# Kernel optimization log

Hardware: AMD Instinct MI355X
Metric: run time of the kernel (lower is better)

Reference implementation:

```python
import jax, jax.numpy as jnp
import numpy as np
from jax import lax

B, N, C, H, W, D, BEV = 2, 6, 64, 128, 352, 48, 64


def _make_buffers():
    # depths: linspace(1,100,D) -> used with shape (1,1,D,1)
    depths = jnp.linspace(1.0, 100.0, D).reshape(1, 1, D, 1)
    y, x = jnp.meshgrid(jnp.arange(H), jnp.arange(W), indexing='ij')
    xy1 = jnp.stack((x.flatten(), y.flatten(), jnp.ones(H * W)), axis=0).astype(jnp.float32)  # (3, H*W)
    return depths, xy1


def setup_inputs() -> dict:
    key = jax.random.key(0)
    ks = jax.random.split(key, 8)
    image_features = jax.random.normal(ks[0], (B * N, C, H, W), jnp.float32)
    # realistic invertible pinhole intrinsics embedded in 4x4
    fx = 500.0 + 10.0 * jax.random.normal(ks[1], (B, N))
    fy = 500.0 + 10.0 * jax.random.normal(ks[2], (B, N))
    K = jnp.tile(jnp.eye(4, dtype=jnp.float32), (B, N, 1, 1))
    K = K.at[..., 0, 0].set(fx).at[..., 1, 1].set(fy)
    K = K.at[..., 0, 2].set(W / 2.0).at[..., 1, 2].set(H / 2.0)
    extrinsics = jnp.tile(jnp.eye(4, dtype=jnp.float32), (B, N, 1, 1)) + 0.01 * jax.random.normal(ks[3], (B, N, 4, 4))
    view_attention = jnp.ones((1, N, 1, H, W), jnp.float32)
    depth_attention = jnp.ones((1, D, 1, 1), jnp.float32)
    # kaiming-normal conv weights (fan_in mode, relu gain sqrt(2))
    c1w = jax.random.normal(ks[4], (BEV, 3, 3, 3), jnp.float32) * np.sqrt(2.0 / (3 * 9))
    c1b = jnp.zeros((BEV,), jnp.float32)
    c2w = jax.random.normal(ks[5], (BEV, BEV, 3, 3), jnp.float32) * np.sqrt(2.0 / (BEV * 9))
    c2b = jnp.zeros((BEV,), jnp.float32)
    bn1_g = jnp.ones((BEV,), jnp.float32); bn1_b = jnp.zeros((BEV,), jnp.float32)
    bn2_g = jnp.ones((BEV,), jnp.float32); bn2_b = jnp.zeros((BEV,), jnp.float32)
    depths, xy1 = _make_buffers()
    return dict(image_features=image_features, intrinsics=K, extrinsics=extrinsics,
                view_attention=view_attention, depth_attention=depth_attention,
                c1w=c1w, c1b=c1b, bn1_g=bn1_g, bn1_b=bn1_b,
                c2w=c2w, c2b=c2b, bn2_g=bn2_g, bn2_b=bn2_b,
                depths=depths, xy1=xy1)


def _conv3x3(x, w, b):
    y = lax.conv_general_dilated(x, w, (1, 1), 'SAME',
                                 dimension_numbers=('NCHW', 'OIHW', 'NCHW'))
    return y + b.reshape(1, -1, 1, 1)


def _bn_train(x, g, b, eps=1e-5):
    # torch BatchNorm2d in training mode: biased batch stats over (B,H,W)
    m = x.mean(axis=(0, 2, 3), keepdims=True)
    v = x.var(axis=(0, 2, 3), keepdims=True)
    return g.reshape(1, -1, 1, 1) * (x - m) * lax.rsqrt(v + eps) + b.reshape(1, -1, 1, 1)


def reference(image_features, intrinsics, extrinsics, view_attention, depth_attention,
              c1w, c1b, bn1_g, bn1_b, c2w, c2b, bn2_g, bn2_b, depths, xy1):
    BN = B * N
    # ---- lift ----
    K3 = intrinsics.reshape(BN, 4, 4)[:, :3, :3]
    Kinv = jnp.linalg.inv(K3)                          # (BN,3,3)
    rays = jnp.einsum('bij,jp->bip', Kinv, xy1)        # (BN,3,H*W)
    # depths (1,1,D,1) * rays (BN,3,1,HW) -> (BN,3,D,HW), then the original's
    # .view(B,N,3,H,W,D) (a raw row-major reshape, reproduced faithfully)
    pc = (depths * rays[:, :, None, :]).reshape(B, N, 3, H, W, D)
    # (depth_probs in the original is computed then discarded; omitted)
    # ---- splat (fused weighted reduction over N and D) ----
    da = jax.nn.softmax(depth_attention, axis=1).reshape(D)       # (D,)
    va = jax.nn.softmax(view_attention, axis=1)[0, :, 0]          # (N,H,W)
    bev_features = jnp.einsum('bnchwd,d,nhw->bchw', pc, da, va)   # (B,3,H,W)
    h = jax.nn.relu(_bn_train(_conv3x3(bev_features, c1w, c1b), bn1_g, bn1_b))
    bev = jax.nn.relu(_bn_train(_conv3x3(h, c2w, c2b), bn2_g, bn2_b))
    return pc, bev
```

## Files before the change

### kernel.cpp

```cpp
#include <hip/hip_runtime.h>

#define W_ 352
#define H_ 128
#define HW 45056
#define D_ 48
#define B_ 2
#define N_ 6
#define DHW (D_*HW)
#define PC_SIZE (36*DHW)
#define BHW (B_*HW)
#define BEVN (B_*64*HW)

#define WS_KINV 0
#define WS_SUM1 192
#define WS_SQ1  256
#define WS_SUM2 448
#define WS_SQ2  512

#define NBN_BLK (BEVN/2048)
#define NPC_BLK (PC_SIZE/1024)

typedef unsigned short ushort_t;
typedef __attribute__((ext_vector_type(8))) short bf16x8;
typedef __attribute__((ext_vector_type(4))) float f32x4;
typedef __attribute__((ext_vector_type(8))) unsigned short u16x8;

static __device__ inline ushort_t f2bf(float f) {
    union { float f; unsigned u; } v; v.f = f;
    unsigned r = v.u + 0x7FFF + ((v.u >> 16) & 1);
    return (ushort_t)(r >> 16);
}
static __device__ inline float bf2f(ushort_t u) {
    union { unsigned u; float f; } v; v.u = ((unsigned)u) << 16; return v.f;
}
static __device__ inline void invert3x3(const float* __restrict__ M, float* __restrict__ o) {
    float a = M[0], b = M[1], c = M[2];
    float d = M[4], e = M[5], f = M[6];
    float g = M[8], h = M[9], ii = M[10];
    float det = a*(e*ii - f*h) - b*(d*ii - f*g) + c*(d*h - e*g);
    float inv = 1.f / det;
    o[0] = (e*ii - f*h)*inv; o[1] = (c*h - b*ii)*inv; o[2] = (b*f - c*e)*inv;
    o[3] = (f*g - d*ii)*inv; o[4] = (a*ii - c*g)*inv; o[5] = (c*d - a*f)*inv;
    o[6] = (d*h - e*g)*inv;  o[7] = (b*g - a*h)*inv;  o[8] = (a*e - b*d)*inv;
}

__global__ __launch_bounds__(256) void k_bevf(const float* __restrict__ K4,
                                              const float* __restrict__ datt,
                                              const float* __restrict__ vatt,
                                              const float* __restrict__ depths,
                                              float* __restrict__ ws,
                                              float* __restrict__ bevf) {
    int t = threadIdx.x;
    if (blockIdx.x == 176) {
        for (int i = 192 + t; i < 640; i += 256) ws[i] = 0.f;
        if (t < 12) invert3x3(K4 + t * 16, ws + WS_KINV + t * 9);
        return;
    }
    __shared__ float sKinv[108], sDa[48], sDep[48];
    if (t < 48) sDep[t] = depths[t];
    if (t >= 192 && t < 204) invert3x3(K4 + (t - 192) * 16, sKinv + (t - 192) * 9);
    if (t == 255) {
        float mx = -1e30f;
        for (int k = 0; k < D_; k++) mx = fmaxf(mx, datt[k]);
        float s = 0.f, e[D_];
        for (int k = 0; k < D_; k++) { e[k] = expf(datt[k] - mx); s += e[k]; }
        float invs = 1.f / s;
        for (int k = 0; k < D_; k++) sDa[k] = e[k] * invs;
    }
    __syncthreads();
    int pix = blockIdx.x * 256 + t;
    float va[N_]; float mx = -1e30f;
    for (int n = 0; n < N_; n++) { va[n] = vatt[n * HW + pix]; mx = fmaxf(mx, va[n]); }
    float s = 0.f;
    for (int n = 0; n < N_; n++) { va[n] = expf(va[n] - mx); s += va[n]; }
    float invs = 1.f / s;
    int q0 = pix * 48;
    int d = q0 / HW;
    int p = q0 - d * HW;
    int y = p / W_;
    int x = p - y * W_;
    float fx = (float)x, fy = (float)y;
    float S0 = 0.f, S1 = 0.f, S2 = 0.f;
    #pragma unroll
    for (int dd = 0; dd < D_; dd++) {
        float wq = sDa[dd] * sDep[d];
        S0 = fmaf(wq, fx, S0);
        S1 = fmaf(wq, fy, S1);
        S2 += wq;
        x++; fx += 1.f;
        if (x == W_) { x = 0; fx = 0.f; y++; fy += 1.f; if (y == H_) { y = 0; fy = 0.f; d++; } }
    }
    for (int b = 0; b < B_; b++) {
        float a0 = 0.f, a1 = 0.f, a2 = 0.f;
        for (int n = 0; n < N_; n++) {
            float van = va[n] * invs;
            const float* kv = sKinv + (b * N_ + n) * 9;
            a0 = fmaf(van, fmaf(kv[0], S0, fmaf(kv[1], S1, kv[2] * S2)), a0);
            a1 = fmaf(van, fmaf(kv[3], S0, fmaf(kv[4], S1, kv[5] * S2)), a1);
            a2 = fmaf(van, fmaf(kv[6], S0, fmaf(kv[7], S1, kv[8] * S2)), a2);
        }
        bevf[(b * 3 + 0) * HW + pix] = a0;
        bevf[(b * 3 + 1) * HW + pix] = a1;
        bevf[(b * 3 + 2) * HW + pix] = a2;
    }
}

__global__ __launch_bounds__(256) void k_conv1(const float* __restrict__ bevf,
                                               const float* __restrict__ w1,
                                               const float* __restrict__ b1,
                                               const float* __restrict__ w2,
                                               ushort_t* __restrict__ h1pm,
                                               ushort_t* __restrict__ packedW) {
    if (blockIdx.x >= 352) {
        int e = (blockIdx.x - 352) * 256 + threadIdx.x;
        int tap = e >> 12;
        int r   = e & 4095;
        int n   = r >> 6, k = r & 63;
        int slot = (k >> 3) ^ (n & 7);
        packedW[tap * 4096 + n * 64 + slot * 8 + (k & 7)] = f2bf(w2[(n * 64 + k) * 9 + tap]);
        return;
    }
    __shared__ float wl[64 * 27];
    for (int i = threadIdx.x; i < 64 * 27; i += 256) wl[i] = w1[i];
    __syncthreads();
    int pix = blockIdx.x * 256 + threadIdx.x;
    int b = pix / HW;
    int rem = pix - b * HW;
    int h = rem / W_;
    int w = rem - h * W_;
    float v[27];
    #pragma unroll
    for (int ci = 0; ci < 3; ci++)
        #pragma unroll
        for (int dy = 0; dy < 3; dy++)
            #pragma unroll
            for (int dx = 0; dx < 3; dx++) {
                int hh = h + dy - 1, ww = w + dx - 1;
                float val = 0.f;
                if (hh >= 0 && hh < H_ && ww >= 0 && ww < W_)
                    val = bevf[(b * 3 + ci) * HW + hh * W_ + ww];
                v[ci * 9 + dy * 3 + dx] = val;
            }
    u16x8 pack[8];
    #pragma unroll
    for (int co = 0; co < 64; co++) {
        float acc = b1[co];
        #pragma unroll
        for (int k = 0; k < 27; k++) acc = fmaf(wl[co * 27 + k], v[k], acc);
        pack[co >> 3][co & 7] = (short)f2bf(acc);
    }
    ushort_t* dst = h1pm + pix * 64;
    #pragma unroll
    for (int j = 0; j < 8; j++)
        *(u16x8*)(dst + j * 8) = pack[j];
}

__global__ __launch_bounds__(256) void k_stats(const ushort_t* __restrict__ x,
                                               float* __restrict__ ws) {
    __shared__ float sSum[64], sSq[64];
    int tid = threadIdx.x;
    if (tid < 64) { sSum[tid] = 0.f; sSq[tid] = 0.f; }
    __syncthreads();
    int c8 = tid & 7;
    int lp = tid >> 3;
    int base = blockIdx.x * 352;
    float s[8] = {0,0,0,0,0,0,0,0}, q[8] = {0,0,0,0,0,0,0,0};
    for (int p = lp; p < 352; p += 32) {
        u16x8 v = *(const u16x8*)(x + (base + p) * 64 + c8 * 8);
        #pragma unroll
        for (int e = 0; e < 8; e++) {
            float f = bf2f(v[e]);
            s[e] += f;
            q[e] = fmaf(f, f, q[e]);
        }
    }
    #pragma unroll
    for (int e = 0; e < 8; e++) {
        s[e] += __shfl_xor(s[e], 8);  s[e] += __shfl_xor(s[e], 16); s[e] += __shfl_xor(s[e], 32);
        q[e] += __shfl_xor(q[e], 8);  q[e] += __shfl_xor(q[e], 16); q[e] += __shfl_xor(q[e], 32);
    }
    if ((tid & 56) == 0) {
        #pragma unroll
        for (int e = 0; e < 8; e++) {
            atomicAdd(&sSum[c8 * 8 + e], s[e]);
            atomicAdd(&sSq[c8 * 8 + e], q[e]);
        }
    }
    __syncthreads();
    if (tid < 64) {
        atomicAdd(ws + WS_SUM1 + tid, sSum[tid]);
        atomicAdd(ws + WS_SQ1 + tid, sSq[tid]);
    }
}

__global__ __launch_bounds__(256) void k_conv2(const ushort_t* __restrict__ h1pm,
                                               const ushort_t* __restrict__ packedW,
                                               const float* __restrict__ b2,
                                               const float* __restrict__ g1,
                                               const float* __restrict__ bb1,
                                               float* __restrict__ ws,
                                               float* __restrict__ h2f) {
    __shared__ __align__(16) ushort_t sA[204 * 64];
    __shared__ __align__(16) ushort_t sB[3 * 4096];
    __shared__ float sSc[64], sSh[64];
    __shared__ float sRs[4][64], sRq[4][64];

    const int tid = threadIdx.x;
    if (tid < 64) {
        const float invM = 1.f / (float)BHW;
        float m = ws[WS_SUM1 + tid] * invM;
        float var = ws[WS_SQ1 + tid] * invM - m * m;
        float sc = g1[tid] * rsqrtf(var + 1e-5f);
        sSc[tid] = sc;
        sSh[tid] = bb1[tid] - m * sc;
    }
    __syncthreads();

    const int b  = blockIdx.z;
    const int x0 = blockIdx.x * 32;
    const int y0 = blockIdx.y * 4;
    const ushort_t* h1p = h1pm + b * HW * 64;

    for (int idx = tid; idx < 204 * 8; idx += 256) {
        int r  = idx >> 3;
        int c8 = idx & 7;
        int hy = r / 34;
        int hx = r - hy * 34;
        int py = y0 + hy - 1, px = x0 + hx - 1;
        u16x8 ov = {0, 0, 0, 0, 0, 0, 0, 0};
        if ((unsigned)py < H_ && (unsigned)px < W_) {
            u16x8 v = *(const u16x8*)(h1p + (py * W_ + px) * 64 + c8 * 8);
            #pragma unroll
            for (int e = 0; e < 8; e++) {
                int ci = c8 * 8 + e;
                float f = fmaxf(fmaf(sSc[ci], bf2f(v[e]), sSh[ci]), 0.f);
                ov[e] = (short)f2bf(f);
            }
        }
        int slot = c8 ^ (r & 7);
        *(u16x8*)(&sA[r * 64 + slot * 8]) = ov;
    }

    const int w    = tid >> 6;
    const int lane = tid & 63;
    const int g    = lane >> 4;
    const int c16  = lane & 15;

    f32x4 acc[2][4];
    #pragma unroll
    for (int m = 0; m < 2; m++)
        #pragma unroll
        for (int n = 0; n < 4; n++)
            acc[m][n] = (f32x4){0.f, 0.f, 0.f, 0.f};

    for (int grp = 0; grp < 3; grp++) {
        __syncthreads();
        const uint4* src = (const uint4*)(packedW + grp * 3 * 4096);
        uint4* dst = (uint4*)sB;
        #pragma unroll
        for (int i = 0; i < 6; i++) dst[tid + 256 * i] = src[tid + 256 * i];
        __syncthreads();
        #pragma unroll
        for (int tt = 0; tt < 3; tt++) {
            bf16x8 afr[2][2];
            #pragma unroll
            for (int mrep = 0; mrep < 2; mrep++)
                #pragma unroll
                for (int kk = 0; kk < 2; kk++) {
                    int r = (w + grp) * 34 + tt + c16 + 16 * mrep;
                    int slot = (g + 4 * kk) ^ (r & 7);
                    afr[mrep][kk] = *(const bf16x8*)(&sA[r * 64 + slot * 8]);
                }
            #pragma unroll
            for (int nrep = 0; nrep < 4; nrep++) {
                int n = 16 * nrep + c16;
                #pragma unroll
                for (int kk = 0; kk < 2; kk++) {
                    int slot = (g + 4 * kk) ^ (n & 7);
                    bf16x8 bfr = *(const bf16x8*)(&sB[tt * 4096 + n * 64 + slot * 8]);
                    #pragma unroll
                    for (int mrep = 0; mrep < 2; mrep++)
                        acc[mrep][nrep] = __builtin_amdgcn_mfma_f32_16x16x32_bf16(
                            afr[mrep][kk], bfr, acc[mrep][nrep], 0, 0, 0);
                }
            }
        }
    }

    const int y = y0 + w;
    #pragma unroll
    for (int nrep = 0; nrep < 4; nrep++) {
        int co = 16 * nrep + c16;
        float bias = b2[co];
        float* dstrow = h2f + (b * 64 + co) * HW + y * W_;
        float s = 0.f, q = 0.f;
        #pragma unroll
        for (int mrep = 0; mrep < 2; mrep++)
            #pragma unroll
            for (int j = 0; j < 4; j++) {
                float val = acc[mrep][nrep][j] + bias;
                s += val;
                q = fmaf(val, val, q);
                dstrow[x0 + 16 * mrep + g * 4 + j] = val;
            }
        s += __shfl_xor(s, 16); s += __shfl_xor(s, 32);
        q += __shfl_xor(q, 16); q += __shfl_xor(q, 32);
        if (g == 0) { sRs[w][co] = s; sRq[w][co] = q; }
    }
    __syncthreads();
    if (tid < 64) {
        float s = sRs[0][tid] + sRs[1][tid] + sRs[2][tid] + sRs[3][tid];
        float q = sRq[0][tid] + sRq[1][tid] + sRq[2][tid] + sRq[3][tid];
        atomicAdd(ws + WS_SUM2 + tid, s);
        atomicAdd(ws + WS_SQ2 + tid, q);
    }
}

__global__ __launch_bounds__(256) void k_tail(const float* __restrict__ depths,
                                              const float* __restrict__ ws,
                                              const float* __restrict__ g2,
                                              const float* __restrict__ bb2,
                                              float* __restrict__ out) {
    int bid = blockIdx.x;
    if (bid < NBN_BLK) {
        float* bev = out + PC_SIZE;
        int t = bid * 256 + threadIdx.x;
        int f = t * 8;
        int c = (f / HW) & 63;
        const float invM = 1.f / (float)BHW;
        float m = ws[WS_SUM2 + c] * invM;
        float var = ws[WS_SQ2 + c] * invM - m * m;
        float sc = g2[c] * rsqrtf(var + 1e-5f);
        float sh = bb2[c] - m * sc;
        f32x4 a = *(f32x4*)(bev + f);
        f32x4 d = *(f32x4*)(bev + f + 4);
        a.x = fmaxf(fmaf(sc, a.x, sh), 0.f);
        a.y = fmaxf(fmaf(sc, a.y, sh), 0.f);
        a.z = fmaxf(fmaf(sc, a.z, sh), 0.f);
        a.w = fmaxf(fmaf(sc, a.w, sh), 0.f);
        d.x = fmaxf(fmaf(sc, d.x, sh), 0.f);
        d.y = fmaxf(fmaf(sc, d.y, sh), 0.f);
        d.z = fmaxf(fmaf(sc, d.z, sh), 0.f);
        d.w = fmaxf(fmaf(sc, d.w, sh), 0.f);
        *(f32x4*)(bev + f) = a;
        *(f32x4*)(bev + f + 4) = d;
    } else {
        int t = (bid - NBN_BLK) * 256 + threadIdx.x;
        int f = t * 4;
        int bnc = f / DHW;
        int r1  = f - bnc * DHW;
        int d   = r1 / HW;
        int p   = r1 - d * HW;
        int y   = p / W_;
        int x   = p - y * W_;
        float ka = ws[WS_KINV + bnc * 3 + 0];
        float kb = ws[WS_KINV + bnc * 3 + 1];
        float kc = ws[WS_KINV + bnc * 3 + 2];
        float dep = depths[d];
        float base = fmaf(kb, (float)y, kc);
        f32x4 v;
        v.x = dep * fmaf(ka, (float)(x + 0), base);
        v.y = dep * fmaf(ka, (float)(x + 1), base);
        v.z = dep * fmaf(ka, (float)(x + 2), base);
        v.w = dep * fmaf(ka, (float)(x + 3), base);
        __builtin_nontemporal_store(v, (f32x4*)(out + f));
    }
}

extern "C" void kernel_launch(void* const* d_in, const int* in_sizes, int n_in,
                              void* d_out, int out_size, void* d_ws, size_t ws_size,
                              hipStream_t stream) {
    const float* K4     = (const float*)d_in[1];
    const float* vatt   = (const float*)d_in[3];
    const float* datt   = (const float*)d_in[4];
    const float* c1w    = (const float*)d_in[5];
    const float* c1b    = (const float*)d_in[6];
    const float* g1     = (const float*)d_in[7];
    const float* bb1    = (const float*)d_in[8];
    const float* c2w    = (const float*)d_in[9];
    const float* c2b    = (const float*)d_in[10];
    const float* g2     = (const float*)d_in[11];
    const float* bb2    = (const float*)d_in[12];
    const float* depths = (const float*)d_in[13];

    float* out = (float*)d_out;
    float* ws  = (float*)d_ws;
    char* base = (char*)d_out;
    ushort_t* h1pm    = (ushort_t*)base;
    float*    bevf    = (float*)(base + (32u << 20));
    ushort_t* packedW = (ushort_t*)(base + (36u << 20));
    float*    h2f     = out + PC_SIZE;

    k_bevf<<<177, 256, 0, stream>>>(K4, datt, vatt, depths, ws, bevf);
    k_conv1<<<496, 256, 0, stream>>>(bevf, c1w, c1b, c2w, h1pm, packedW);
    k_stats<<<256, 256, 0, stream>>>(h1pm, ws);
    k_conv2<<<dim3(11, 32, 2), 256, 0, stream>>>(h1pm, packedW, c2b, g1, bb1, ws, h2f);
    k_tail<<<NBN_BLK + NPC_BLK, 256, 0, stream>>>(depths, ws, g2, bb2, out);
}
```

Measured before the change: 129.9 us.

## Spread point-cloud writes across all kernels to overlap with compute stages

The large point-cloud output write, previously done entirely in the final tail kernel, is split into chunks and appended as extra blocks to each of the five kernels. Each pc block inverts its camera's intrinsics itself, so it no longer depends on the workspace. Scratch buffers move into the last slice of the pc region, which the tail kernel writes last. The aim is to hide the memory-bound pc stores behind the compute-bound conv and stats stages, at the cost of redundant per-thread 3x3 inversions and bandwidth contention with those stages.

```diff
diff --git a/kernel.cpp b/kernel.cpp
--- a/kernel.cpp
+++ b/kernel.cpp
@@ -11,14 +11,19 @@
 #define BHW (B_*HW)
 #define BEVN (B_*64*HW)
 
-#define WS_KINV 0
 #define WS_SUM1 192
 #define WS_SQ1  256
 #define WS_SUM2 448
 #define WS_SQ2  512
 
 #define NBN_BLK (BEVN/2048)
-#define NPC_BLK (PC_SIZE/1024)
+#define SCRATCH_F 4194304
+#define PCA_TOT ((PC_SIZE - SCRATCH_F)/1024)
+#define PCA1 22000
+#define PCA2 20000
+#define PCA3 18000
+#define PCA4 (PCA_TOT - PCA1 - PCA2 - PCA3)
+#define TAILPC (SCRATCH_F/1024)
 
 typedef unsigned short ushort_t;
 typedef __attribute__((ext_vector_type(8))) short bf16x8;
@@ -44,16 +49,49 @@
     o[6] = (d*h - e*g)*inv;  o[7] = (b*g - a*h)*inv;  o[8] = (a*e - b*d)*inv;
 }
 
+static __device__ inline void pc_write(int pcblk, const float* __restrict__ K4,
+                                       const float* __restrict__ depths,
+                                       float* __restrict__ out) {
+    int f = pcblk * 1024 + (int)threadIdx.x * 4;
+    int bnc = f / DHW;
+    int r1  = f - bnc * DHW;
+    int d   = r1 / HW;
+    int p   = r1 - d * HW;
+    int y   = p / W_;
+    int x   = p - y * W_;
+    int bn  = bnc / 3;
+    int rr  = bnc - bn * 3;
+    const float* M = K4 + bn * 16;
+    float a = M[0], b = M[1], c = M[2];
+    float dd = M[4], e = M[5], ff = M[6];
+    float g = M[8], h = M[9], i = M[10];
+    float det = a*(e*i - ff*h) + b*(ff*g - dd*i) + c*(dd*h - e*g);
+    float inv = 1.f / det;
+    float ka, kb, kc;
+    if (rr == 0)      { ka = (e*i - ff*h)*inv;  kb = (c*h - b*i)*inv;  kc = (b*ff - c*e)*inv; }
+    else if (rr == 1) { ka = (ff*g - dd*i)*inv; kb = (a*i - c*g)*inv;  kc = (c*dd - a*ff)*inv; }
+    else              { ka = (dd*h - e*g)*inv;  kb = (b*g - a*h)*inv;  kc = (a*e - b*dd)*inv; }
+    float dep = depths[d];
+    float base = fmaf(kb, (float)y, kc);
+    f32x4 v;
+    v.x = dep * fmaf(ka, (float)(x + 0), base);
+    v.y = dep * fmaf(ka, (float)(x + 1), base);
+    v.z = dep * fmaf(ka, (float)(x + 2), base);
+    v.w = dep * fmaf(ka, (float)(x + 3), base);
+    __builtin_nontemporal_store(v, (f32x4*)(out + f));
+}
+
 __global__ __launch_bounds__(256) void k_bevf(const float* __restrict__ K4,
                                               const float* __restrict__ datt,
                                               const float* __restrict__ vatt,
                                               const float* __restrict__ depths,
                                               float* __restrict__ ws,
-                                              float* __restrict__ bevf) {
-    int t = threadIdx.x;
-    if (blockIdx.x == 176) {
+                                              float* __restrict__ bevf,
+                                              float* __restrict__ out) {
+    int bid = blockIdx.x, t = threadIdx.x;
+    if (bid >= 177) { pc_write(bid - 177, K4, depths, out); return; }
+    if (bid == 176) {
         for (int i = 192 + t; i < 640; i += 256) ws[i] = 0.f;
-        if (t < 12) invert3x3(K4 + t * 16, ws + WS_KINV + t * 9);
         return;
     }
     __shared__ float sKinv[108], sDa[48], sDep[48];
@@ -68,7 +106,7 @@
         for (int k = 0; k < D_; k++) sDa[k] = e[k] * invs;
     }
     __syncthreads();
-    int pix = blockIdx.x * 256 + t;
+    int pix = bid * 256 + t;
     float va[N_]; float mx = -1e30f;
     for (int n = 0; n < N_; n++) { va[n] = vatt[n * HW + pix]; mx = fmaxf(mx, va[n]); }
     float s = 0.f;
@@ -110,9 +148,14 @@
                                                const float* __restrict__ b1,
                                                const float* __restrict__ w2,
                                                ushort_t* __restrict__ h1pm,
-                                               ushort_t* __restrict__ packedW) {
-    if (blockIdx.x >= 352) {
-        int e = (blockIdx.x - 352) * 256 + threadIdx.x;
+                                               ushort_t* __restrict__ packedW,
+                                               const float* __restrict__ K4,
+                                               const float* __restrict__ depths,
+                                               float* __restrict__ out) {
+    int bid = blockIdx.x;
+    if (bid >= 496) { pc_write(bid - 496 + PCA1, K4, depths, out); return; }
+    if (bid >= 352) {
+        int e = (bid - 352) * 256 + threadIdx.x;
         int tap = e >> 12;
         int r   = e & 4095;
         int n   = r >> 6, k = r & 63;
@@ -123,7 +166,7 @@
     __shared__ float wl[64 * 27];
     for (int i = threadIdx.x; i < 64 * 27; i += 256) wl[i] = w1[i];
     __syncthreads();
-    int pix = blockIdx.x * 256 + threadIdx.x;
+    int pix = bid * 256 + threadIdx.x;
     int b = pix / HW;
     int rem = pix - b * HW;
     int h = rem / W_;
@@ -156,14 +199,19 @@
 }
 
 __global__ __launch_bounds__(256) void k_stats(const ushort_t* __restrict__ x,
-                                               float* __restrict__ ws) {
+                                               float* __restrict__ ws,
+                                               const float* __restrict__ K4,
+                                               const float* __restrict__ depths,
+                                               float* __restrict__ out) {
+    int bid = blockIdx.x;
+    if (bid >= 256) { pc_write(bid - 256 + PCA1 + PCA2, K4, depths, out); return; }
     __shared__ float sSum[64], sSq[64];
     int tid = threadIdx.x;
     if (tid < 64) { sSum[tid] = 0.f; sSq[tid] = 0.f; }
     __syncthreads();
     int c8 = tid & 7;
     int lp = tid >> 3;
-    int base = blockIdx.x * 352;
+    int base = bid * 352;
     float s[8] = {0,0,0,0,0,0,0,0}, q[8] = {0,0,0,0,0,0,0,0};
     for (int p = lp; p < 352; p += 32) {
         u16x8 v = *(const u16x8*)(x + (base + p) * 64 + c8 * 8);
@@ -199,7 +247,13 @@
                                                const float* __restrict__ g1,
                                                const float* __restrict__ bb1,
                                                float* __restrict__ ws,
-                                               float* __restrict__ h2f) {
+                                               float* __restrict__ h2f,
+                                               const float* __restrict__ K4,
+                                               const float* __restrict__ depths,
+                                               float* __restrict__ out) {
+    int bid = blockIdx.x;
+    if (bid >= 704) { pc_write(bid - 704 + PCA1 + PCA2 + PCA3, K4, depths, out); return; }
+
     __shared__ __align__(16) ushort_t sA[204 * 64];
     __shared__ __align__(16) ushort_t sB[3 * 4096];
     __shared__ float sSc[64], sSh[64];
@@ -216,9 +270,12 @@
     }
     __syncthreads();
 
-    const int b  = blockIdx.z;
-    const int x0 = blockIdx.x * 32;
-    const int y0 = blockIdx.y * 4;
+    const int b  = bid / 352;
+    const int r0 = bid - b * 352;
+    const int yb = r0 / 11;
+    const int xb = r0 - yb * 11;
+    const int x0 = xb * 32;
+    const int y0 = yb * 4;
     const ushort_t* h1p = h1pm + b * HW * 64;
 
     for (int idx = tid; idx < 204 * 8; idx += 256) {
@@ -320,51 +377,31 @@
                                               const float* __restrict__ ws,
                                               const float* __restrict__ g2,
                                               const float* __restrict__ bb2,
+                                              const float* __restrict__ K4,
                                               float* __restrict__ out) {
     int bid = blockIdx.x;
-    if (bid < NBN_BLK) {
-        float* bev = out + PC_SIZE;
-        int t = bid * 256 + threadIdx.x;
-        int f = t * 8;
-        int c = (f / HW) & 63;
-        const float invM = 1.f / (float)BHW;
-        float m = ws[WS_SUM2 + c] * invM;
-        float var = ws[WS_SQ2 + c] * invM - m * m;
-        float sc = g2[c] * rsqrtf(var + 1e-5f);
-        float sh = bb2[c] - m * sc;
-        f32x4 a = *(f32x4*)(bev + f);
-        f32x4 d = *(f32x4*)(bev + f + 4);
-        a.x = fmaxf(fmaf(sc, a.x, sh), 0.f);
-        a.y = fmaxf(fmaf(sc, a.y, sh), 0.f);
-        a.z = fmaxf(fmaf(sc, a.z, sh), 0.f);
-        a.w = fmaxf(fmaf(sc, a.w, sh), 0.f);
-        d.x = fmaxf(fmaf(sc, d.x, sh), 0.f);
-        d.y = fmaxf(fmaf(sc, d.y, sh), 0.f);
-        d.z = fmaxf(fmaf(sc, d.z, sh), 0.f);
-        d.w = fmaxf(fmaf(sc, d.w, sh), 0.f);
-        *(f32x4*)(bev + f) = a;
-        *(f32x4*)(bev + f + 4) = d;
-    } else {
-        int t = (bid - NBN_BLK) * 256 + threadIdx.x;
-        int f = t * 4;
-        int bnc = f / DHW;
-        int r1  = f - bnc * DHW;
-        int d   = r1 / HW;
-        int p   = r1 - d * HW;
-        int y   = p / W_;
-        int x   = p - y * W_;
-        float ka = ws[WS_KINV + bnc * 3 + 0];
-        float kb = ws[WS_KINV + bnc * 3 + 1];
-        float kc = ws[WS_KINV + bnc * 3 + 2];
-        float dep = depths[d];
-        float base = fmaf(kb, (float)y, kc);
-        f32x4 v;
-        v.x = dep * fmaf(ka, (float)(x + 0), base);
-        v.y = dep * fmaf(ka, (float)(x + 1), base);
-        v.z = dep * fmaf(ka, (float)(x + 2), base);
-        v.w = dep * fmaf(ka, (float)(x + 3), base);
-        __builtin_nontemporal_store(v, (f32x4*)(out + f));
-    }
+    if (bid >= NBN_BLK) { pc_write(bid - NBN_BLK + PCA_TOT, K4, depths, out); return; }
+    float* bev = out + PC_SIZE;
+    int t = bid * 256 + threadIdx.x;
+    int f = t * 8;
+    int c = (f / HW) & 63;
+    const float invM = 1.f / (float)BHW;
+    float m = ws[WS_SUM2 + c] * invM;
+    float var = ws[WS_SQ2 + c] * invM - m * m;
+    float sc = g2[c] * rsqrtf(var + 1e-5f);
+    float sh = bb2[c] - m * sc;
+    f32x4 a = *(f32x4*)(bev + f);
+    f32x4 d = *(f32x4*)(bev + f + 4);
+    a.x = fmaxf(fmaf(sc, a.x, sh), 0.f);
+    a.y = fmaxf(fmaf(sc, a.y, sh), 0.f);
+    a.z = fmaxf(fmaf(sc, a.z, sh), 0.f);
+    a.w = fmaxf(fmaf(sc, a.w, sh), 0.f);
+    d.x = fmaxf(fmaf(sc, d.x, sh), 0.f);
+    d.y = fmaxf(fmaf(sc, d.y, sh), 0.f);
+    d.z = fmaxf(fmaf(sc, d.z, sh), 0.f);
+    d.w = fmaxf(fmaf(sc, d.w, sh), 0.f);
+    *(f32x4*)(bev + f) = a;
+    *(f32x4*)(bev + f + 4) = d;
 }
 
 extern "C" void kernel_launch(void* const* d_in, const int* in_sizes, int n_in,
@@ -385,15 +422,15 @@
 
     float* out = (float*)d_out;
     float* ws  = (float*)d_ws;
-    char* base = (char*)d_out;
-    ushort_t* h1pm    = (ushort_t*)base;
-    float*    bevf    = (float*)(base + (32u << 20));
-    ushort_t* packedW = (ushort_t*)(base + (36u << 20));
+    char* sbase = (char*)d_out + (size_t)(PC_SIZE - SCRATCH_F) * 4;
+    ushort_t* h1pm    = (ushort_t*)sbase;
+    float*    bevf    = (float*)(sbase + (12u << 20));
+    ushort_t* packedW = (ushort_t*)(sbase + (14u << 20));
     float*    h2f     = out + PC_SIZE;
 
-    k_bevf<<<177, 256, 0, stream>>>(K4, datt, vatt, depths, ws, bevf);
-    k_conv1<<<496, 256, 0, stream>>>(bevf, c1w, c1b, c2w, h1pm, packedW);
-    k_stats<<<256, 256, 0, stream>>>(h1pm, ws);
-    k_conv2<<<dim3(11, 32, 2), 256, 0, stream>>>(h1pm, packedW, c2b, g1, bb1, ws, h2f);
-    k_tail<<<NBN_BLK + NPC_BLK, 256, 0, stream>>>(depths, ws, g2, bb2, out);
-}
+    k_bevf <<<177 + PCA1, 256, 0, stream>>>(K4, datt, vatt, depths, ws, bevf, out);
+    k_conv1<<<496 + PCA2, 256, 0, stream>>>(bevf, c1w, c1b, c2w, h1pm, packedW, K4, depths, out);
+    k_stats<<<256 + PCA3, 256, 0, stream>>>(h1pm, ws, K4, depths, out);
+    k_conv2<<<704 + PCA4, 256, 0, stream>>>(h1pm, packedW, c2b, g1, bb1, ws, h2f, K4, depths, out);
+    k_tail <<<NBN_BLK + TAILPC, 256, 0, stream>>>(depths, ws, g2, bb2, K4, out);
+}
```

Result: slower. 136.6 us (+5.2%).

## Fuse BEV feature computation into conv1 tiles and widen point-cloud stores

Applied to the files above, without the earlier changes.

The separate BEV-feature kernel is merged into the first convolution: each 8x32 tile computes its haloed BEV features directly into shared memory, so the bevf intermediate buffer and one launch go away. The point-cloud writer in the tail kernel now writes eight floats per thread and computes the K-inverse row inline instead of reading it from the workspace. Halo recomputation adds some redundant per-pixel softmax and depth-sum work, and conv2 switches to a flattened 1D grid.

```diff
diff --git a/kernel.cpp b/kernel.cpp
--- a/kernel.cpp
+++ b/kernel.cpp
@@ -11,14 +11,13 @@
 #define BHW (B_*HW)
 #define BEVN (B_*64*HW)
 
-#define WS_KINV 0
 #define WS_SUM1 192
 #define WS_SQ1  256
 #define WS_SUM2 448
 #define WS_SQ2  512
 
 #define NBN_BLK (BEVN/2048)
-#define NPC_BLK (PC_SIZE/1024)
+#define NPC_BLK (PC_SIZE/2048)
 
 typedef unsigned short ushort_t;
 typedef __attribute__((ext_vector_type(8))) short bf16x8;
@@ -44,22 +43,78 @@
     o[6] = (d*h - e*g)*inv;  o[7] = (b*g - a*h)*inv;  o[8] = (a*e - b*d)*inv;
 }
 
-__global__ __launch_bounds__(256) void k_bevf(const float* __restrict__ K4,
-                                              const float* __restrict__ datt,
-                                              const float* __restrict__ vatt,
-                                              const float* __restrict__ depths,
-                                              float* __restrict__ ws,
-                                              float* __restrict__ bevf) {
-    int t = threadIdx.x;
-    if (blockIdx.x == 176) {
-        for (int i = 192 + t; i < 640; i += 256) ws[i] = 0.f;
-        if (t < 12) invert3x3(K4 + t * 16, ws + WS_KINV + t * 9);
+static __device__ inline void pc_write8(int pcblk, const float* __restrict__ K4,
+                                        const float* __restrict__ depths,
+                                        float* __restrict__ out) {
+    int f = pcblk * 2048 + (int)threadIdx.x * 8;
+    int bnc = f / DHW;
+    int r1  = f - bnc * DHW;
+    int d   = r1 / HW;
+    int p   = r1 - d * HW;
+    int y   = p / W_;
+    int x   = p - y * W_;
+    int bn  = bnc / 3;
+    int rr  = bnc - bn * 3;
+    const float* M = K4 + bn * 16;
+    float a = M[0], b = M[1], c = M[2];
+    float dd = M[4], e = M[5], ff = M[6];
+    float g = M[8], h = M[9], i = M[10];
+    float det = a*(e*i - ff*h) + b*(ff*g - dd*i) + c*(dd*h - e*g);
+    float inv = 1.f / det;
+    float ka, kb, kc;
+    if (rr == 0)      { ka = (e*i - ff*h)*inv;  kb = (c*h - b*i)*inv;  kc = (b*ff - c*e)*inv; }
+    else if (rr == 1) { ka = (ff*g - dd*i)*inv; kb = (a*i - c*g)*inv;  kc = (c*dd - a*ff)*inv; }
+    else              { ka = (dd*h - e*g)*inv;  kb = (b*g - a*h)*inv;  kc = (a*e - b*dd)*inv; }
+    float dep = depths[d];
+    float base = fmaf(kb, (float)y, kc);
+    f32x4 v0, v1;
+    v0.x = dep * fmaf(ka, (float)(x + 0), base);
+    v0.y = dep * fmaf(ka, (float)(x + 1), base);
+    v0.z = dep * fmaf(ka, (float)(x + 2), base);
+    v0.w = dep * fmaf(ka, (float)(x + 3), base);
+    v1.x = dep * fmaf(ka, (float)(x + 4), base);
+    v1.y = dep * fmaf(ka, (float)(x + 5), base);
+    v1.z = dep * fmaf(ka, (float)(x + 6), base);
+    v1.w = dep * fmaf(ka, (float)(x + 7), base);
+    __builtin_nontemporal_store(v0, (f32x4*)(out + f));
+    __builtin_nontemporal_store(v1, (f32x4*)(out + f + 4));
+}
+
+__global__ __launch_bounds__(256) void k_fused1(const float* __restrict__ K4,
+                                                const float* __restrict__ datt,
+                                                const float* __restrict__ vatt,
+                                                const float* __restrict__ depths,
+                                                const float* __restrict__ w1,
+                                                const float* __restrict__ b1,
+                                                const float* __restrict__ w2,
+                                                float* __restrict__ ws,
+                                                ushort_t* __restrict__ h1pm,
+                                                ushort_t* __restrict__ packedW) {
+    int bid = blockIdx.x, tid = threadIdx.x;
+    if (bid >= 352) {
+        int e = (bid - 352) * 256 + tid;
+        int tap = e >> 12;
+        int r   = e & 4095;
+        int n   = r >> 6, k = r & 63;
+        int slot = (k >> 3) ^ (n & 7);
+        packedW[tap * 4096 + n * 64 + slot * 8 + (k & 7)] = f2bf(w2[(n * 64 + k) * 9 + tap]);
         return;
     }
-    __shared__ float sKinv[108], sDa[48], sDep[48];
-    if (t < 48) sDep[t] = depths[t];
-    if (t >= 192 && t < 204) invert3x3(K4 + (t - 192) * 16, sKinv + (t - 192) * 9);
-    if (t == 255) {
+    if (bid == 0) {
+        for (int i = 192 + tid; i < 576; i += 256) ws[i] = 0.f;
+    }
+    __shared__ float sBev[3][10][34];
+    __shared__ float wl[64 * 27];
+    __shared__ float sDep[48], sDa[48], sKinv[54];
+
+    int b  = bid / 176;
+    int t0 = bid - b * 176;
+    int ty = t0 / 11, tx = t0 - ty * 11;
+    int y0 = ty * 8, x0 = tx * 32;
+
+    if (tid < 48) sDep[tid] = depths[tid];
+    if (tid >= 64 && tid < 70) invert3x3(K4 + (b * 6 + tid - 64) * 16, sKinv + (tid - 64) * 9);
+    if (tid == 192) {
         float mx = -1e30f;
         for (int k = 0; k < D_; k++) mx = fmaxf(mx, datt[k]);
         float s = 0.f, e[D_];
@@ -67,80 +122,60 @@
         float invs = 1.f / s;
         for (int k = 0; k < D_; k++) sDa[k] = e[k] * invs;
     }
-    __syncthreads();
-    int pix = blockIdx.x * 256 + t;
-    float va[N_]; float mx = -1e30f;
-    for (int n = 0; n < N_; n++) { va[n] = vatt[n * HW + pix]; mx = fmaxf(mx, va[n]); }
-    float s = 0.f;
-    for (int n = 0; n < N_; n++) { va[n] = expf(va[n] - mx); s += va[n]; }
-    float invs = 1.f / s;
-    int q0 = pix * 48;
-    int d = q0 / HW;
-    int p = q0 - d * HW;
-    int y = p / W_;
-    int x = p - y * W_;
-    float fx = (float)x, fy = (float)y;
-    float S0 = 0.f, S1 = 0.f, S2 = 0.f;
-    #pragma unroll
-    for (int dd = 0; dd < D_; dd++) {
-        float wq = sDa[dd] * sDep[d];
-        S0 = fmaf(wq, fx, S0);
-        S1 = fmaf(wq, fy, S1);
-        S2 += wq;
-        x++; fx += 1.f;
-        if (x == W_) { x = 0; fx = 0.f; y++; fy += 1.f; if (y == H_) { y = 0; fy = 0.f; d++; } }
-    }
-    for (int b = 0; b < B_; b++) {
+    for (int i = tid; i < 64 * 27; i += 256) wl[i] = w1[i];
+    __syncthreads();
+
+    for (int idx = tid; idx < 340; idx += 256) {
+        int hy = idx / 34, hx = idx - hy * 34;
+        int py = y0 + hy - 1, px = x0 + hx - 1;
         float a0 = 0.f, a1 = 0.f, a2 = 0.f;
-        for (int n = 0; n < N_; n++) {
-            float van = va[n] * invs;
-            const float* kv = sKinv + (b * N_ + n) * 9;
-            a0 = fmaf(van, fmaf(kv[0], S0, fmaf(kv[1], S1, kv[2] * S2)), a0);
-            a1 = fmaf(van, fmaf(kv[3], S0, fmaf(kv[4], S1, kv[5] * S2)), a1);
-            a2 = fmaf(van, fmaf(kv[6], S0, fmaf(kv[7], S1, kv[8] * S2)), a2);
+        if ((unsigned)py < H_ && (unsigned)px < W_) {
+            int pix = py * W_ + px;
+            float va[N_]; float mx = -1e30f;
+            for (int n = 0; n < N_; n++) { va[n] = vatt[n * HW + pix]; mx = fmaxf(mx, va[n]); }
+            float s = 0.f;
+            for (int n = 0; n < N_; n++) { va[n] = expf(va[n] - mx); s += va[n]; }
+            float invs = 1.f / s;
+            int q0 = pix * 48;
+            int d = q0 / HW;
+            int p = q0 - d * HW;
+            int y = p / W_;
+            int x = p - y * W_;
+            float fx = (float)x, fy = (float)y;
+            float S0 = 0.f, S1 = 0.f, S2 = 0.f;
+            #pragma unroll
+            for (int dd = 0; dd < D_; dd++) {
+                float wq = sDa[dd] * sDep[d];
+                S0 = fmaf(wq, fx, S0);
+                S1 = fmaf(wq, fy, S1);
+                S2 += wq;
+                x++; fx += 1.f;
+                if (x == W_) { x = 0; fx = 0.f; y++; fy += 1.f; if (y == H_) { y = 0; fy = 0.f; d++; } }
+            }
+            for (int n = 0; n < N_; n++) {
+                float van = va[n] * invs;
+                const float* kv = sKinv + n * 9;
+                a0 = fmaf(van, fmaf(kv[0], S0, fmaf(kv[1], S1, kv[2] * S2)), a0);
+                a1 = fmaf(van, fmaf(kv[3], S0, fmaf(kv[4], S1, kv[5] * S2)), a1);
+                a2 = fmaf(van, fmaf(kv[6], S0, fmaf(kv[7], S1, kv[8] * S2)), a2);
+            }
         }
-        bevf[(b * 3 + 0) * HW + pix] = a0;
-        bevf[(b * 3 + 1) * HW + pix] = a1;
-        bevf[(b * 3 + 2) * HW + pix] = a2;
-    }
-}
-
-__global__ __launch_bounds__(256) void k_conv1(const float* __restrict__ bevf,
-                                               const float* __restrict__ w1,
-                                               const float* __restrict__ b1,
-                                               const float* __restrict__ w2,
-                                               ushort_t* __restrict__ h1pm,
-                                               ushort_t* __restrict__ packedW) {
-    if (blockIdx.x >= 352) {
-        int e = (blockIdx.x - 352) * 256 + threadIdx.x;
-        int tap = e >> 12;
-        int r   = e & 4095;
-        int n   = r >> 6, k = r & 63;
-        int slot = (k >> 3) ^ (n & 7);
-        packedW[tap * 4096 + n * 64 + slot * 8 + (k & 7)] = f2bf(w2[(n * 64 + k) * 9 + tap]);
-        return;
-    }
-    __shared__ float wl[64 * 27];
-    for (int i = threadIdx.x; i < 64 * 27; i += 256) wl[i] = w1[i];
-    __syncthreads();
-    int pix = blockIdx.x * 256 + threadIdx.x;
-    int b = pix / HW;
-    int rem = pix - b * HW;
-    int h = rem / W_;
-    int w = rem - h * W_;
+        sBev[0][hy][hx] = a0;
+        sBev[1][hy][hx] = a1;
+        sBev[2][hy][hx] = a2;
+    }
+    __syncthreads();
+
+    int oy = tid >> 5, ox = tid & 31;
+    int y = y0 + oy, x = x0 + ox;
     float v[27];
     #pragma unroll
     for (int ci = 0; ci < 3; ci++)
         #pragma unroll
         for (int dy = 0; dy < 3; dy++)
             #pragma unroll
-            for (int dx = 0; dx < 3; dx++) {
-                int hh = h + dy - 1, ww = w + dx - 1;
-                float val = 0.f;
-                if (hh >= 0 && hh < H_ && ww >= 0 && ww < W_)
-                    val = bevf[(b * 3 + ci) * HW + hh * W_ + ww];
-                v[ci * 9 + dy * 3 + dx] = val;
-            }
+            for (int dx = 0; dx < 3; dx++)
+                v[ci * 9 + dy * 3 + dx] = sBev[ci][oy + dy][ox + dx];
     u16x8 pack[8];
     #pragma unroll
     for (int co = 0; co < 64; co++) {
@@ -149,7 +184,7 @@
         for (int k = 0; k < 27; k++) acc = fmaf(wl[co * 27 + k], v[k], acc);
         pack[co >> 3][co & 7] = (short)f2bf(acc);
     }
-    ushort_t* dst = h1pm + pix * 64;
+    ushort_t* dst = h1pm + (size_t)(b * HW + y * W_ + x) * 64;
     #pragma unroll
     for (int j = 0; j < 8; j++)
         *(u16x8*)(dst + j * 8) = pack[j];
@@ -166,7 +201,7 @@
     int base = blockIdx.x * 352;
     float s[8] = {0,0,0,0,0,0,0,0}, q[8] = {0,0,0,0,0,0,0,0};
     for (int p = lp; p < 352; p += 32) {
-        u16x8 v = *(const u16x8*)(x + (base + p) * 64 + c8 * 8);
+        u16x8 v = *(const u16x8*)(x + (size_t)(base + p) * 64 + c8 * 8);
         #pragma unroll
         for (int e = 0; e < 8; e++) {
             float f = bf2f(v[e]);
@@ -216,10 +251,14 @@
     }
     __syncthreads();
 
-    const int b  = blockIdx.z;
-    const int x0 = blockIdx.x * 32;
-    const int y0 = blockIdx.y * 4;
-    const ushort_t* h1p = h1pm + b * HW * 64;
+    const int bid = blockIdx.x;
+    const int b  = bid / 352;
+    const int r0 = bid - b * 352;
+    const int yb = r0 / 11;
+    const int xb = r0 - yb * 11;
+    const int x0 = xb * 32;
+    const int y0 = yb * 4;
+    const ushort_t* h1p = h1pm + (size_t)b * HW * 64;
 
     for (int idx = tid; idx < 204 * 8; idx += 256) {
         int r  = idx >> 3;
@@ -229,7 +268,7 @@
         int py = y0 + hy - 1, px = x0 + hx - 1;
         u16x8 ov = {0, 0, 0, 0, 0, 0, 0, 0};
         if ((unsigned)py < H_ && (unsigned)px < W_) {
-            u16x8 v = *(const u16x8*)(h1p + (py * W_ + px) * 64 + c8 * 8);
+            u16x8 v = *(const u16x8*)(h1p + (size_t)(py * W_ + px) * 64 + c8 * 8);
             #pragma unroll
             for (int e = 0; e < 8; e++) {
                 int ci = c8 * 8 + e;
@@ -292,7 +331,7 @@
     for (int nrep = 0; nrep < 4; nrep++) {
         int co = 16 * nrep + c16;
         float bias = b2[co];
-        float* dstrow = h2f + (b * 64 + co) * HW + y * W_;
+        float* dstrow = h2f + (size_t)(b * 64 + co) * HW + y * W_;
         float s = 0.f, q = 0.f;
         #pragma unroll
         for (int mrep = 0; mrep < 2; mrep++)
@@ -320,51 +359,31 @@
                                               const float* __restrict__ ws,
                                               const float* __restrict__ g2,
                                               const float* __restrict__ bb2,
+                                              const float* __restrict__ K4,
                                               float* __restrict__ out) {
     int bid = blockIdx.x;
-    if (bid < NBN_BLK) {
-        float* bev = out + PC_SIZE;
-        int t = bid * 256 + threadIdx.x;
-        int f = t * 8;
-        int c = (f / HW) & 63;
-        const float invM = 1.f / (float)BHW;
-        float m = ws[WS_SUM2 + c] * invM;
-        float var = ws[WS_SQ2 + c] * invM - m * m;
-        float sc = g2[c] * rsqrtf(var + 1e-5f);
-        float sh = bb2[c] - m * sc;
-        f32x4 a = *(f32x4*)(bev + f);
-        f32x4 d = *(f32x4*)(bev + f + 4);
-        a.x = fmaxf(fmaf(sc, a.x, sh), 0.f);
-        a.y = fmaxf(fmaf(sc, a.y, sh), 0.f);
-        a.z = fmaxf(fmaf(sc, a.z, sh), 0.f);
-        a.w = fmaxf(fmaf(sc, a.w, sh), 0.f);
-        d.x = fmaxf(fmaf(sc, d.x, sh), 0.f);
-        d.y = fmaxf(fmaf(sc, d.y, sh), 0.f);
-        d.z = fmaxf(fmaf(sc, d.z, sh), 0.f);
-        d.w = fmaxf(fmaf(sc, d.w, sh), 0.f);
-        *(f32x4*)(bev + f) = a;
-        *(f32x4*)(bev + f + 4) = d;
-    } else {
-        int t = (bid - NBN_BLK) * 256 + threadIdx.x;
-        int f = t * 4;
-        int bnc = f / DHW;
-        int r1  = f - bnc * DHW;
-        int d   = r1 / HW;
-        int p   = r1 - d * HW;
-        int y   = p / W_;
-        int x   = p - y * W_;
-        float ka = ws[WS_KINV + bnc * 3 + 0];
-        float kb = ws[WS_KINV + bnc * 3 + 1];
-        float kc = ws[WS_KINV + bnc * 3 + 2];
-        float dep = depths[d];
-        float base = fmaf(kb, (float)y, kc);
-        f32x4 v;
-        v.x = dep * fmaf(ka, (float)(x + 0), base);
-        v.y = dep * fmaf(ka, (float)(x + 1), base);
-        v.z = dep * fmaf(ka, (float)(x + 2), base);
-        v.w = dep * fmaf(ka, (float)(x + 3), base);
-        __builtin_nontemporal_store(v, (f32x4*)(out + f));
-    }
+    if (bid >= NBN_BLK) { pc_write8(bid - NBN_BLK, K4, depths, out); return; }
+    float* bev = out + PC_SIZE;
+    int t = bid * 256 + threadIdx.x;
+    int f = t * 8;
+    int c = (f / HW) & 63;
+    const float invM = 1.f / (float)BHW;
+    float m = ws[WS_SUM2 + c] * invM;
+    float var = ws[WS_SQ2 + c] * invM - m * m;
+    float sc = g2[c] * rsqrtf(var + 1e-5f);
+    float sh = bb2[c] - m * sc;
+    f32x4 a = *(f32x4*)(bev + f);
+    f32x4 d = *(f32x4*)(bev + f + 4);
+    a.x = fmaxf(fmaf(sc, a.x, sh), 0.f);
+    a.y = fmaxf(fmaf(sc, a.y, sh), 0.f);
+    a.z = fmaxf(fmaf(sc, a.z, sh), 0.f);
+    a.w = fmaxf(fmaf(sc, a.w, sh), 0.f);
+    d.x = fmaxf(fmaf(sc, d.x, sh), 0.f);
+    d.y = fmaxf(fmaf(sc, d.y, sh), 0.f);
+    d.z = fmaxf(fmaf(sc, d.z, sh), 0.f);
+    d.w = fmaxf(fmaf(sc, d.w, sh), 0.f);
+    *(f32x4*)(bev + f) = a;
+    *(f32x4*)(bev + f + 4) = d;
 }
 
 extern "C" void kernel_launch(void* const* d_in, const int* in_sizes, int n_in,
@@ -387,13 +406,11 @@
     float* ws  = (float*)d_ws;
     char* base = (char*)d_out;
     ushort_t* h1pm    = (ushort_t*)base;
-    float*    bevf    = (float*)(base + (32u << 20));
-    ushort_t* packedW = (ushort_t*)(base + (36u << 20));
+    ushort_t* packedW = (ushort_t*)(base + (12u << 20));
     float*    h2f     = out + PC_SIZE;
 
-    k_bevf<<<177, 256, 0, stream>>>(K4, datt, vatt, depths, ws, bevf);
-    k_conv1<<<496, 256, 0, stream>>>(bevf, c1w, c1b, c2w, h1pm, packedW);
-    k_stats<<<256, 256, 0, stream>>>(h1pm, ws);
-    k_conv2<<<dim3(11, 32, 2), 256, 0, stream>>>(h1pm, packedW, c2b, g1, bb1, ws, h2f);
-    k_tail<<<NBN_BLK + NPC_BLK, 256, 0, stream>>>(depths, ws, g2, bb2, out);
-}
+    k_fused1<<<496, 256, 0, stream>>>(K4, datt, vatt, depths, c1w, c1b, c2w, ws, h1pm, packedW);
+    k_stats <<<256, 256, 0, stream>>>(h1pm, ws);
+    k_conv2 <<<704, 256, 0, stream>>>(h1pm, packedW, c2b, g1, bb1, ws, h2f);
+    k_tail  <<<NBN_BLK + NPC_BLK, 256, 0, stream>>>(depths, ws, g2, bb2, K4, out);
+}
```

Result: slower. 200.3 us (+54.2%).
